# Optimization experiments

Measured on AMD Instinct MI355X. Metric: run time of the kernel, lower is better.

Reference implementation:

```python
import jax, jax.numpy as jnp
import numpy as np

B, S, D = 8, 1024, 512


def setup_inputs() -> dict:
    key = jax.random.key(0)
    k1, k2, k3, k4, k5, k6, k7 = jax.random.split(key, 7)
    inp = jax.random.normal(k1, (B, S, D), dtype=jnp.float32)
    aspect = jax.random.normal(k2, (B, S, D), dtype=jnp.float32)
    # lengths in [S//2, S], with max exactly S (the module requires max(len)==S)
    inp_len = jax.random.randint(k3, (B,), S // 2, S + 1).astype(jnp.float32)
    inp_len = inp_len.at[0].set(float(S))
    lim = float(np.sqrt(6.0 / (D + D)))  # xavier_uniform bound
    w1 = jax.random.uniform(k4, (D, D), jnp.float32, -lim, lim)
    b1 = jax.random.uniform(k5, (D,), jnp.float32, -lim, lim)
    w2 = jax.random.uniform(k6, (D, D), jnp.float32, -lim, lim)
    b2 = jax.random.uniform(k7, (D,), jnp.float32, -lim, lim)
    return {"inp": inp, "inp_len": inp_len, "aspect": aspect,
            "w1": w1, "b1": b1, "w2": w2, "b2": b2}


def reference(inp, inp_len, aspect, w1, b1, w2, b2):
    # inp, aspect: [B,S,D]; inp_len: [B] float lengths with max == S
    Bv, Sv, Dv = inp.shape
    scale = jnp.sqrt(inp_len)[:, None, None]                      # [B,1,1]
    att = jnp.einsum('bsd,btd->bst', aspect, inp) / scale          # [B,S,S]
    # mask over the query (row) dimension, as in the original expand
    mask = (jnp.arange(Sv)[None, :] < inp_len.astype(jnp.int32)[:, None]).astype(inp.dtype)  # [B,S]
    exp = att * mask[:, :, None]
    att_n = exp / (jnp.sum(exp, axis=-1, keepdims=True) + 1e-4)    # linear (non-exp) normalize
    weighted = jnp.einsum('bst,btd->bsd', att_n, inp)              # [B,S,D]
    ffn_inp = weighted + (inp + aspect) * mask[:, :, None]
    # FFN: two square linears with relu, plus inner residual
    o1 = jax.nn.relu(jnp.einsum('bsd,ed->bse', ffn_inp, w1) + b1)
    o2 = jax.nn.relu(jnp.einsum('bsd,ed->bse', o1, w2) + b2)
    ffn_out = o2 + ffn_inp
    final = ffn_inp + ffn_out
    return final / jnp.linalg.norm(final, axis=2, keepdims=True)
```

## Files before the change

kernel.cpp:

```cpp
#include <hip/hip_runtime.h>

#define Bq 8
#define Sq 1024
#define Dq 512

typedef __attribute__((ext_vector_type(8))) short bf16x8;
typedef __attribute__((ext_vector_type(4))) float f32x4;

__device__ __forceinline__ unsigned short f2bf(float f) {
  unsigned int u = __float_as_uint(f);
  return (unsigned short)((u + 0x7fffu + ((u >> 16) & 1u)) >> 16);
}

__device__ __forceinline__ void load_lds16(const unsigned short* g, unsigned short* l) {
  __builtin_amdgcn_global_load_lds(
      (const __attribute__((address_space(1))) unsigned int*)g,
      (__attribute__((address_space(3))) unsigned int*)l, 16, 0, 0);
}


__global__ __launch_bounds__(256) void prep_t(
    const float* __restrict__ inp,
    unsigned short* __restrict__ inpT, float* __restrict__ partial) {
  __shared__ unsigned short tile[64][66];
  __shared__ float csum[16][64];
  int idx = blockIdx.x;
  int tid = threadIdx.x;
  int b = idx & 7, tt = (idx >> 3) & 15, dd = idx >> 7;
  int r = tid >> 4, c4 = (tid & 15) * 4;
  const float* src = inp + ((size_t)b * Sq + tt * 64) * Dq + dd * 64;
  float cp0 = 0.f, cp1 = 0.f, cp2 = 0.f, cp3 = 0.f;
#pragma unroll
  for (int p = 0; p < 4; ++p) {
    float4 v = *(const float4*)(src + (size_t)(r + p * 16) * Dq + c4);
    ushort4 o; o.x = f2bf(v.x); o.y = f2bf(v.y); o.z = f2bf(v.z); o.w = f2bf(v.w);
    *(ushort4*)&tile[r + p * 16][c4] = o;
    cp0 += v.x; cp1 += v.y; cp2 += v.z; cp3 += v.w;
  }
  csum[r][c4] = cp0; csum[r][c4 + 1] = cp1; csum[r][c4 + 2] = cp2; csum[r][c4 + 3] = cp3;
  __syncthreads();
  unsigned short* dst = inpT + (size_t)b * Dq * Sq + (size_t)dd * 64 * Sq + tt * 64;
#pragma unroll
  for (int p = 0; p < 4; ++p) {
    int d = (tid >> 4) + p * 16;
    int tq = (tid & 15) * 4;
    ushort4 o;
    o.x = tile[tq][d]; o.y = tile[tq + 1][d]; o.z = tile[tq + 2][d]; o.w = tile[tq + 3][d];
    *(ushort4*)(dst + (size_t)d * Sq + tq) = o;
  }
  if (tid < 64) {
    float s = 0.f;
#pragma unroll
    for (int rr = 0; rr < 16; ++rr) s += csum[rr][tid];
    partial[((size_t)b * 16 + tt) * Dq + dd * 64 + tid] = s;
  }
}

__global__ __launch_bounds__(256, 5) void gram_fac(
    const unsigned short* __restrict__ inpT, const float* __restrict__ partial,
    const float* __restrict__ aspect, const float* __restrict__ lenv,
    const float* __restrict__ w1, const float* __restrict__ w2,
    unsigned short* __restrict__ Gm, float* __restrict__ fac,
    unsigned short* __restrict__ asp_bf,
    unsigned short* __restrict__ w1b, unsigned short* __restrict__ w2b) {
  __shared__ unsigned short sA[2][32 * 64];
  __shared__ unsigned short sB[2][64 * 64];
  int idx = blockIdx.x;
  int tid = threadIdx.x;
  int lane = tid & 63, wave = tid >> 6;

  if (idx >= 2048) {
    int blk = idx - 2048;
    const float* src = (blk < 256) ? w1 : w2;
    unsigned short* dst = (blk < 256) ? w1b : w2b;
    int li = ((blk & 255) * 256 + tid) * 4;
    int n = li >> 9, k = li & 511;
    float4 v = *(const float4*)(src + li);
    ushort4 o; o.x = f2bf(v.x); o.y = f2bf(v.y); o.z = f2bf(v.z); o.w = f2bf(v.w);
    int x = ((k >> 3) & 3) ^ ((n >> 1) & 3);
    int off = (k >> 5) * 16384 + n * 32 + x * 8 + (k & 7);
    *(ushort4*)(dst + off) = o;
    return;
  }
  if (idx >= 1536) {
    int blk = idx - 1536;
    const float* s = aspect + (size_t)blk * 8192 + tid * 4;
    unsigned short* d = asp_bf + (size_t)blk * 8192 + tid * 4;
#pragma unroll
    for (int j = 0; j < 8; ++j) {
      float4 v = *(const float4*)(s + j * 1024);
      ushort4 o; o.x = f2bf(v.x); o.y = f2bf(v.y); o.z = f2bf(v.z); o.w = f2bf(v.w);
      *(ushort4*)(d + j * 1024) = o;
    }
    return;
  }
  if (idx >= 1024) {
    float* cs = (float*)sA;
    int fblk = idx - 1024;
    int b = fblk >> 6;
    int s0 = (fblk & 63) * 16;
#pragma unroll
    for (int h = 0; h < 2; ++h) {
      int d = h * 256 + tid;
      float s = 0.f;
      const float* p = partial + (size_t)b * 16 * Dq + d;
#pragma unroll
      for (int t = 0; t < 16; ++t) s += p[t * Dq];
      cs[d] = s;
    }
    __syncthreads();
    int g = lane >> 4, lr = lane & 15;
    int row = s0 + wave * 4 + g;
    const float* a = aspect + ((size_t)b * Sq + row) * Dq + lr * 32;
    float sum = 0.f;
#pragma unroll
    for (int j = 0; j < 8; ++j) {
      float4 v = *(const float4*)(a + j * 4);
      const float* c = cs + lr * 32 + j * 4;
      sum += v.x * c[0] + v.y * c[1] + v.z * c[2] + v.w * c[3];
    }
#pragma unroll
    for (int off = 1; off < 16; off <<= 1) sum += __shfl_xor(sum, off, 64);
    if (lr == 0) {
      float len = lenv[b];
      float scale = sqrtf(len);
      float f = 0.f;
      if (row < (int)len) f = 1.f / (scale * (sum / scale + 1e-4f));
      fac[b * Sq + row] = f;
    }
    return;
  }

  const int K = 1024;
  int b = idx & 7;
  int tile = idx >> 3;
  int bm = tile & 15, bn = tile >> 4;
  const unsigned short* Ab = inpT + (size_t)b * Dq * Sq + (size_t)bm * 32 * K;
  const unsigned short* Bb = inpT + (size_t)b * Dq * Sq + (size_t)bn * 64 * K;
  int lr = lane & 15, lq = lane >> 4;
  int x7 = lr & 7;
  int l3 = lane >> 3, l7 = lane & 7;

  const unsigned short* gA = Ab + (size_t)(wave * 8 + l3) * K + (l7 ^ l3) * 8;
  const unsigned short* gB = Bb + (size_t)(wave * 16 + l3) * K + (l7 ^ l3) * 8;
  int dbaseA = (wave * 64 + lane) * 8;
  int dbaseB0 = (wave * 128 + lane) * 8;
  int dbaseB1 = (wave * 128 + 64 + lane) * 8;

  f32x4 acc[2] = {};

  auto issue = [&](int buf, int k0) {
    load_lds16(gA + k0, &sA[buf][dbaseA]);
    load_lds16(gB + k0, &sB[buf][dbaseB0]);
    load_lds16(gB + (size_t)8 * K + k0, &sB[buf][dbaseB1]);
  };

  int wm = (wave & 1) * 16, wn = (wave >> 1) * 32;
  issue(0, 0);
#pragma unroll
  for (int it = 0; it < 16; ++it) {
    int cur = it & 1;
    if (it + 1 < 16) {
      issue(cur ^ 1, (it + 1) << 6);
      asm volatile("s_waitcnt vmcnt(3)" ::: "memory");
    } else {
      asm volatile("s_waitcnt vmcnt(0)" ::: "memory");
    }
    __builtin_amdgcn_s_barrier();
#pragma unroll
    for (int c = 0; c < 2; ++c) {
      int g = c * 4 + lq;
      bf16x8 a0 = *(const bf16x8*)&sA[cur][((wm + lr) * 8 + (g ^ x7)) * 8];
      bf16x8 b0 = *(const bf16x8*)&sB[cur][((wn + lr) * 8 + (g ^ x7)) * 8];
      bf16x8 b1 = *(const bf16x8*)&sB[cur][((wn + 16 + lr) * 8 + (g ^ x7)) * 8];
      acc[0] = __builtin_amdgcn_mfma_f32_16x16x32_bf16(a0, b0, acc[0], 0, 0, 0);
      acc[1] = __builtin_amdgcn_mfma_f32_16x16x32_bf16(a0, b1, acc[1], 0, 0, 0);
    }
    asm volatile("s_waitcnt lgkmcnt(0)" ::: "memory");
    __builtin_amdgcn_sched_barrier(0);
    __builtin_amdgcn_s_barrier();
  }

  unsigned short* sP = sA[0];
#pragma unroll
  for (int ni = 0; ni < 2; ++ni)
#pragma unroll
    for (int i = 0; i < 4; ++i) {
      int rl = wm + lq * 4 + i;
      int ccl = wn + ni * 16 + lr;
      int x = (rl >> 3) ^ ((ccl >> 1) & 3);
      sP[ccl * 32 + x * 8 + (rl & 7)] = f2bf(acc[ni][i]);
    }
  __syncthreads();
  unsigned short* Ob = Gm + (size_t)b * 512 * 512 + (size_t)bm * 16384 + (size_t)bn * 2048;
  *(bf16x8*)(Ob + tid * 8) = *(const bf16x8*)(sP + tid * 8);
}

__global__ __launch_bounds__(512, 2) void mega_ffn(
    const unsigned short* __restrict__ aspb, const unsigned short* __restrict__ G,
    const unsigned short* __restrict__ w1b, const unsigned short* __restrict__ w2b,
    const float* __restrict__ b1, const float* __restrict__ b2,
    const float* __restrict__ inp, const float* __restrict__ aspect,
    const float* __restrict__ fac, const float* __restrict__ lenv,
    float* __restrict__ out) {
  __shared__ unsigned short ldsA[32 * 512];
  __shared__ float ssqW[8 * 32];
  int tid = threadIdx.x;
  int lane = tid & 63, wave = tid >> 6;
  int lr = lane & 15, lq = lane >> 4;
  int batch = blockIdx.x & 7;
  int pos = blockIdx.x >> 3;
  int r0 = batch * 1024 + pos * 32;
  int c0 = wave * 64;

  f32x4 acc[2][4];
  float ffnv[2][4][4];

  auto aoff = [&](int rr, int c) {
    int cq = c >> 3;
    return rr * 512 + ((cq ^ (rr & 7)) << 3) + (c & 7);
  };
  auto baddr = [&](const unsigned short* Bp, int kc, int cc) {
    return Bp + kc * 16384 + cc * 32 + ((lq ^ ((cc >> 1) & 3)) << 3);
  };

  auto gemmPhase = [&](const unsigned short* Bp) {
    bf16x8 bq[3][4];
    bf16x8 aq[2][2];
#pragma unroll
    for (int m = 0; m < 2; ++m)
#pragma unroll
      for (int t = 0; t < 4; ++t) acc[m][t] = (f32x4){0.f, 0.f, 0.f, 0.f};
#pragma unroll
    for (int t = 0; t < 4; ++t) {
      bq[0][t] = *(const bf16x8*)baddr(Bp, 0, c0 + t * 16 + lr);
      bq[1][t] = *(const bf16x8*)baddr(Bp, 1, c0 + t * 16 + lr);
    }
#pragma unroll
    for (int m = 0; m < 2; ++m)
      aq[0][m] = *(const bf16x8*)&ldsA[aoff(m * 16 + lr, lq * 8)];
#pragma unroll
    for (int kc = 0; kc < 16; ++kc) {
      if (kc + 2 < 16) {
#pragma unroll
        for (int t = 0; t < 4; ++t)
          bq[(kc + 2) % 3][t] = *(const bf16x8*)baddr(Bp, kc + 2, c0 + t * 16 + lr);
      }
      if (kc + 1 < 16) {
#pragma unroll
        for (int m = 0; m < 2; ++m)
          aq[(kc + 1) & 1][m] =
              *(const bf16x8*)&ldsA[aoff(m * 16 + lr, (kc + 1) * 32 + lq * 8)];
      }
      __builtin_amdgcn_s_setprio(1);
#pragma unroll
      for (int t = 0; t < 4; ++t) {
        acc[0][t] = __builtin_amdgcn_mfma_f32_16x16x32_bf16(aq[kc & 1][0], bq[kc % 3][t],
                                                            acc[0][t], 0, 0, 0);
        acc[1][t] = __builtin_amdgcn_mfma_f32_16x16x32_bf16(aq[kc & 1][1], bq[kc % 3][t],
                                                            acc[1][t], 0, 0, 0);
      }
      __builtin_amdgcn_s_setprio(0);
    }
  };

#pragma unroll
  for (int h = 0; h < 8; ++h) {
    int s = h * 512 + tid;
    int rr = s >> 6, sq = s & 63;
    int cq = sq ^ (rr & 7);
    load_lds16(aspb + (size_t)(r0 + rr) * 512 + cq * 8, ldsA + s * 8);
  }
  asm volatile("s_waitcnt vmcnt(0)" ::: "memory");
  __syncthreads();

  gemmPhase(G + (size_t)batch * 512 * 512);
  int len = (int)lenv[batch];
  float facv[2][4];
#pragma unroll
  for (int m = 0; m < 2; ++m)
#pragma unroll
    for (int i = 0; i < 4; ++i) facv[m][i] = fac[r0 + m * 16 + lq * 4 + i];
  __syncthreads();
#pragma unroll
  for (int m = 0; m < 2; ++m)
#pragma unroll
    for (int t = 0; t < 4; ++t)
#pragma unroll
      for (int i = 0; i < 4; ++i) {
        int rr = m * 16 + lq * 4 + i;
        int gr = r0 + rr;
        size_t idx = (size_t)gr * 512 + c0 + t * 16 + lr;
        float add = ((gr & 1023) < len) ? (inp[idx] + aspect[idx]) : 0.f;
        float v = acc[m][t][i] * facv[m][i] + add;
        ffnv[m][t][i] = v;
        ldsA[aoff(rr, c0 + t * 16 + lr)] = f2bf(v);
      }
  __syncthreads();

  gemmPhase(w1b);
  float biasv[4];
#pragma unroll
  for (int t = 0; t < 4; ++t) biasv[t] = b1[c0 + t * 16 + lr];
  __syncthreads();
#pragma unroll
  for (int m = 0; m < 2; ++m)
#pragma unroll
    for (int t = 0; t < 4; ++t)
#pragma unroll
      for (int i = 0; i < 4; ++i) {
        int rr = m * 16 + lq * 4 + i;
        ldsA[aoff(rr, c0 + t * 16 + lr)] = f2bf(fmaxf(acc[m][t][i] + biasv[t], 0.f));
      }
  __syncthreads();

  gemmPhase(w2b);
#pragma unroll
  for (int t = 0; t < 4; ++t) biasv[t] = b2[c0 + t * 16 + lr];
  float ssq[2][4] = {{0.f, 0.f, 0.f, 0.f}, {0.f, 0.f, 0.f, 0.f}};
#pragma unroll
  for (int m = 0; m < 2; ++m)
#pragma unroll
    for (int t = 0; t < 4; ++t)
#pragma unroll
      for (int i = 0; i < 4; ++i) {
        float v = 2.f * ffnv[m][t][i] + fmaxf(acc[m][t][i] + biasv[t], 0.f);
        ffnv[m][t][i] = v;
        ssq[m][i] += v * v;
      }
#pragma unroll
  for (int off = 1; off < 16; off <<= 1)
#pragma unroll
    for (int m = 0; m < 2; ++m)
#pragma unroll
      for (int i = 0; i < 4; ++i) ssq[m][i] += __shfl_xor(ssq[m][i], off, 64);
  if (lr == 0)
#pragma unroll
    for (int m = 0; m < 2; ++m)
#pragma unroll
      for (int i = 0; i < 4; ++i) ssqW[wave * 32 + m * 16 + lq * 4 + i] = ssq[m][i];
  __syncthreads();
  float rn[2][4];
#pragma unroll
  for (int m = 0; m < 2; ++m)
#pragma unroll
    for (int i = 0; i < 4; ++i) {
      float s = 0.f;
#pragma unroll
      for (int w = 0; w < 8; ++w) s += ssqW[w * 32 + m * 16 + lq * 4 + i];
      rn[m][i] = 1.f / sqrtf(s);
    }
#pragma unroll
  for (int m = 0; m < 2; ++m)
#pragma unroll
    for (int t = 0; t < 4; ++t)
#pragma unroll
      for (int i = 0; i < 4; ++i) {
        int gr = r0 + m * 16 + lq * 4 + i;
        out[(size_t)gr * 512 + c0 + t * 16 + lr] = ffnv[m][t][i] * rn[m][i];
      }
}

extern "C" void kernel_launch(void* const* d_in, const int* in_sizes, int n_in,
                              void* d_out, int out_size, void* d_ws, size_t ws_size,
                              hipStream_t stream) {
  const float* inp = (const float*)d_in[0];
  const float* inp_len = (const float*)d_in[1];
  const float* aspect = (const float*)d_in[2];
  const float* w1 = (const float*)d_in[3];
  const float* b1 = (const float*)d_in[4];
  const float* w2 = (const float*)d_in[5];
  const float* b2 = (const float*)d_in[6];
  float* out = (float*)d_out;

  char* W = (char*)d_ws;
  const size_t MB = 1ull << 20;
  unsigned short* asp_bf = (unsigned short*)(W + 0);
  unsigned short* inpT   = (unsigned short*)(W + 8 * MB);
  unsigned short* Gm     = (unsigned short*)(W + 16 * MB);
  unsigned short* w1bf   = (unsigned short*)(W + 20 * MB);
  unsigned short* w2bf   = (unsigned short*)(W + 20 * MB + 512 * 1024);
  float*          partial= (float*)(W + 21 * MB);
  float*          fac    = (float*)(W + 22 * MB);

  prep_t<<<1024, 256, 0, stream>>>(inp, inpT, partial);

  gram_fac<<<2560, 256, 0, stream>>>(inpT, partial, aspect, inp_len, w1, w2,
                                     Gm, fac, asp_bf, w1bf, w2bf);

  mega_ffn<<<256, 512, 0, stream>>>(
      asp_bf, Gm, w1bf, w2bf, b1, b2, inp, aspect, fac, inp_len, out);
}
```

Measured before the change: 130.3 us.

## Enlarge Gram GEMM tiles to 64x128 with 512-thread blocks and remap side tasks

```diff
diff --git a/kernel.cpp b/kernel.cpp
--- a/kernel.cpp
+++ b/kernel.cpp
@@ -56,24 +56,24 @@
   }
 }
 
-__global__ __launch_bounds__(256, 5) void gram_fac(
+__global__ __launch_bounds__(512, 2) void gram_fac(
     const unsigned short* __restrict__ inpT, const float* __restrict__ partial,
     const float* __restrict__ aspect, const float* __restrict__ lenv,
     const float* __restrict__ w1, const float* __restrict__ w2,
     unsigned short* __restrict__ Gm, float* __restrict__ fac,
     unsigned short* __restrict__ asp_bf,
     unsigned short* __restrict__ w1b, unsigned short* __restrict__ w2b) {
-  __shared__ unsigned short sA[2][32 * 64];
-  __shared__ unsigned short sB[2][64 * 64];
+  __shared__ unsigned short sA[2][64 * 64];
+  __shared__ unsigned short sB[2][128 * 64];
   int idx = blockIdx.x;
   int tid = threadIdx.x;
   int lane = tid & 63, wave = tid >> 6;
 
-  if (idx >= 2048) {
-    int blk = idx - 2048;
-    const float* src = (blk < 256) ? w1 : w2;
-    unsigned short* dst = (blk < 256) ? w1b : w2b;
-    int li = ((blk & 255) * 256 + tid) * 4;
+  if (idx >= 768) {
+    int blk = idx - 768;
+    const float* src = (blk < 128) ? w1 : w2;
+    unsigned short* dst = (blk < 128) ? w1b : w2b;
+    int li = ((blk & 127) * 512 + tid) * 4;
     int n = li >> 9, k = li & 511;
     float4 v = *(const float4*)(src + li);
     ushort4 o; o.x = f2bf(v.x); o.y = f2bf(v.y); o.z = f2bf(v.z); o.w = f2bf(v.w);
@@ -82,26 +82,25 @@
     *(ushort4*)(dst + off) = o;
     return;
   }
-  if (idx >= 1536) {
-    int blk = idx - 1536;
-    const float* s = aspect + (size_t)blk * 8192 + tid * 4;
-    unsigned short* d = asp_bf + (size_t)blk * 8192 + tid * 4;
+  if (idx >= 512) {
+    int blk = idx - 512;
+    const float* s = aspect + (size_t)blk * 16384 + tid * 4;
+    unsigned short* d = asp_bf + (size_t)blk * 16384 + tid * 4;
 #pragma unroll
     for (int j = 0; j < 8; ++j) {
-      float4 v = *(const float4*)(s + j * 1024);
+      float4 v = *(const float4*)(s + j * 2048);
       ushort4 o; o.x = f2bf(v.x); o.y = f2bf(v.y); o.z = f2bf(v.z); o.w = f2bf(v.w);
-      *(ushort4*)(d + j * 1024) = o;
+      *(ushort4*)(d + j * 2048) = o;
     }
     return;
   }
-  if (idx >= 1024) {
+  if (idx >= 256) {
     float* cs = (float*)sA;
-    int fblk = idx - 1024;
-    int b = fblk >> 6;
-    int s0 = (fblk & 63) * 16;
-#pragma unroll
-    for (int h = 0; h < 2; ++h) {
-      int d = h * 256 + tid;
+    int fblk = idx - 256;
+    int b = fblk >> 5;
+    int s0 = (fblk & 31) * 32;
+    {
+      int d = tid;
       float s = 0.f;
       const float* p = partial + (size_t)b * 16 * Dq + d;
 #pragma unroll
@@ -134,28 +133,27 @@
   const int K = 1024;
   int b = idx & 7;
   int tile = idx >> 3;
-  int bm = tile & 15, bn = tile >> 4;
-  const unsigned short* Ab = inpT + (size_t)b * Dq * Sq + (size_t)bm * 32 * K;
-  const unsigned short* Bb = inpT + (size_t)b * Dq * Sq + (size_t)bn * 64 * K;
+  int bm = tile & 7, bn = tile >> 3;
+  const unsigned short* Ab = inpT + (size_t)b * Dq * Sq + (size_t)bm * 64 * K;
+  const unsigned short* Bb = inpT + (size_t)b * Dq * Sq + (size_t)bn * 128 * K;
   int lr = lane & 15, lq = lane >> 4;
   int x7 = lr & 7;
-  int l3 = lane >> 3, l7 = lane & 7;
-
-  const unsigned short* gA = Ab + (size_t)(wave * 8 + l3) * K + (l7 ^ l3) * 8;
-  const unsigned short* gB = Bb + (size_t)(wave * 16 + l3) * K + (l7 ^ l3) * 8;
-  int dbaseA = (wave * 64 + lane) * 8;
-  int dbaseB0 = (wave * 128 + lane) * 8;
-  int dbaseB1 = (wave * 128 + 64 + lane) * 8;
-
-  f32x4 acc[2] = {};
+  int t8 = tid >> 3, t7 = tid & 7;
+
+  const unsigned short* gA = Ab + (size_t)t8 * K + (t7 ^ (t8 & 7)) * 8;
+  const unsigned short* gB = Bb + (size_t)t8 * K + (t7 ^ (t8 & 7)) * 8;
+  const unsigned short* gB2 = Bb + (size_t)(t8 + 64) * K + (t7 ^ (t8 & 7)) * 8;
+  int dbase = tid * 8;
+
+  f32x4 acc[2][2] = {};
 
   auto issue = [&](int buf, int k0) {
-    load_lds16(gA + k0, &sA[buf][dbaseA]);
-    load_lds16(gB + k0, &sB[buf][dbaseB0]);
-    load_lds16(gB + (size_t)8 * K + k0, &sB[buf][dbaseB1]);
+    load_lds16(gA + k0, &sA[buf][dbase]);
+    load_lds16(gB + k0, &sB[buf][dbase]);
+    load_lds16(gB2 + k0, &sB[buf][4096 + dbase]);
   };
 
-  int wm = (wave & 1) * 16, wn = (wave >> 1) * 32;
+  int wm = (wave & 1) * 32, wn = (wave >> 1) * 32;
   issue(0, 0);
 #pragma unroll
   for (int it = 0; it < 16; ++it) {
@@ -169,31 +167,40 @@
     __builtin_amdgcn_s_barrier();
 #pragma unroll
     for (int c = 0; c < 2; ++c) {
-      int g = c * 4 + lq;
-      bf16x8 a0 = *(const bf16x8*)&sA[cur][((wm + lr) * 8 + (g ^ x7)) * 8];
-      bf16x8 b0 = *(const bf16x8*)&sB[cur][((wn + lr) * 8 + (g ^ x7)) * 8];
-      bf16x8 b1 = *(const bf16x8*)&sB[cur][((wn + 16 + lr) * 8 + (g ^ x7)) * 8];
-      acc[0] = __builtin_amdgcn_mfma_f32_16x16x32_bf16(a0, b0, acc[0], 0, 0, 0);
-      acc[1] = __builtin_amdgcn_mfma_f32_16x16x32_bf16(a0, b1, acc[1], 0, 0, 0);
+      int g = (c * 4 + lq) ^ x7;
+      bf16x8 a0 = *(const bf16x8*)&sA[cur][((wm + lr) * 8 + g) * 8];
+      bf16x8 a1 = *(const bf16x8*)&sA[cur][((wm + 16 + lr) * 8 + g) * 8];
+      bf16x8 b0 = *(const bf16x8*)&sB[cur][((wn + lr) * 8 + g) * 8];
+      bf16x8 b1 = *(const bf16x8*)&sB[cur][((wn + 16 + lr) * 8 + g) * 8];
+      acc[0][0] = __builtin_amdgcn_mfma_f32_16x16x32_bf16(a0, b0, acc[0][0], 0, 0, 0);
+      acc[0][1] = __builtin_amdgcn_mfma_f32_16x16x32_bf16(a0, b1, acc[0][1], 0, 0, 0);
+      acc[1][0] = __builtin_amdgcn_mfma_f32_16x16x32_bf16(a1, b0, acc[1][0], 0, 0, 0);
+      acc[1][1] = __builtin_amdgcn_mfma_f32_16x16x32_bf16(a1, b1, acc[1][1], 0, 0, 0);
     }
     asm volatile("s_waitcnt lgkmcnt(0)" ::: "memory");
     __builtin_amdgcn_sched_barrier(0);
     __builtin_amdgcn_s_barrier();
   }
 
-  unsigned short* sP = sA[0];
-#pragma unroll
-  for (int ni = 0; ni < 2; ++ni)
-#pragma unroll
-    for (int i = 0; i < 4; ++i) {
-      int rl = wm + lq * 4 + i;
-      int ccl = wn + ni * 16 + lr;
-      int x = (rl >> 3) ^ ((ccl >> 1) & 3);
-      sP[ccl * 32 + x * 8 + (rl & 7)] = f2bf(acc[ni][i]);
-    }
-  __syncthreads();
-  unsigned short* Ob = Gm + (size_t)b * 512 * 512 + (size_t)bm * 16384 + (size_t)bn * 2048;
-  *(bf16x8*)(Ob + tid * 8) = *(const bf16x8*)(sP + tid * 8);
+  unsigned short* sP = sB[0];
+  int kcl = wm >> 5;
+#pragma unroll
+  for (int mi = 0; mi < 2; ++mi)
+#pragma unroll
+    for (int ni = 0; ni < 2; ++ni)
+#pragma unroll
+      for (int i = 0; i < 4; ++i) {
+        int rl = mi * 16 + lq * 4 + i;
+        int nl = wn + ni * 16 + lr;
+        int x = (rl >> 3) ^ ((nl >> 1) & 3);
+        sP[kcl * 4096 + nl * 32 + x * 8 + (rl & 7)] = f2bf(acc[mi][ni][i]);
+      }
+  __syncthreads();
+  unsigned short* Ob = Gm + (size_t)b * 512 * 512 + (size_t)(bm * 2) * 16384 +
+                       (size_t)bn * 4096;
+#pragma unroll
+  for (int h = 0; h < 2; ++h)
+    *(bf16x8*)(Ob + h * 16384 + tid * 8) = *(const bf16x8*)(sP + h * 4096 + tid * 8);
 }
 
 __global__ __launch_bounds__(512, 2) void mega_ffn(
@@ -385,7 +392,7 @@
 
   prep_t<<<1024, 256, 0, stream>>>(inp, inpT, partial);
 
-  gram_fac<<<2560, 256, 0, stream>>>(inpT, partial, aspect, inp_len, w1, w2,
+  gram_fac<<<1024, 512, 0, stream>>>(inpT, partial, aspect, inp_len, w1, w2,
                                      Gm, fac, asp_bf, w1bf, w2bf);
 
   mega_ffn<<<256, 512, 0, stream>>>(
```

Result: no change. 132.1 us (+1.3%).

## Stage FFN weight tiles through a triple-buffered LDS ring via async loads

Applied to the files above, without the earlier changes.

```diff
diff --git a/kernel.cpp b/kernel.cpp
--- a/kernel.cpp
+++ b/kernel.cpp
@@ -196,15 +196,19 @@
   *(bf16x8*)(Ob + tid * 8) = *(const bf16x8*)(sP + tid * 8);
 }
 
-__global__ __launch_bounds__(512, 2) void mega_ffn(
+#define MEGA_SMEM (32768 + 3 * 32768 + 1024)
+
+__global__ __launch_bounds__(512, 1) void mega_ffn(
     const unsigned short* __restrict__ aspb, const unsigned short* __restrict__ G,
     const unsigned short* __restrict__ w1b, const unsigned short* __restrict__ w2b,
     const float* __restrict__ b1, const float* __restrict__ b2,
     const float* __restrict__ inp, const float* __restrict__ aspect,
     const float* __restrict__ fac, const float* __restrict__ lenv,
     float* __restrict__ out) {
-  __shared__ unsigned short ldsA[32 * 512];
-  __shared__ float ssqW[8 * 32];
+  extern __shared__ char smem[];
+  unsigned short* ldsA = (unsigned short*)smem;
+  unsigned short* wbuf = (unsigned short*)(smem + 32768);
+  float* ssqW = (float*)(smem + 32768 + 3 * 32768);
   int tid = threadIdx.x;
   int lane = tid & 63, wave = tid >> 6;
   int lr = lane & 15, lq = lane >> 4;
@@ -220,52 +224,52 @@
     int cq = c >> 3;
     return rr * 512 + ((cq ^ (rr & 7)) << 3) + (c & 7);
   };
-  auto baddr = [&](const unsigned short* Bp, int kc, int cc) {
-    return Bp + kc * 16384 + cc * 32 + ((lq ^ ((cc >> 1) & 3)) << 3);
+  int bx = (lq ^ ((lr >> 1) & 3)) * 8;
+  int rdbase = (c0 + lr) * 32 + bx;
+
+  auto stage = [&](int buf, int kc, const unsigned short* Bp) {
+    const unsigned short* src = Bp + kc * 16384 + wave * 2048 + lane * 8;
+    unsigned short* dst = wbuf + buf * 16384 + wave * 2048 + lane * 8;
+#pragma unroll
+    for (int i = 0; i < 4; ++i) load_lds16(src + i * 512, dst + i * 512);
   };
 
   auto gemmPhase = [&](const unsigned short* Bp) {
-    bf16x8 bq[3][4];
-    bf16x8 aq[2][2];
 #pragma unroll
     for (int m = 0; m < 2; ++m)
 #pragma unroll
       for (int t = 0; t < 4; ++t) acc[m][t] = (f32x4){0.f, 0.f, 0.f, 0.f};
-#pragma unroll
-    for (int t = 0; t < 4; ++t) {
-      bq[0][t] = *(const bf16x8*)baddr(Bp, 0, c0 + t * 16 + lr);
-      bq[1][t] = *(const bf16x8*)baddr(Bp, 1, c0 + t * 16 + lr);
-    }
-#pragma unroll
-    for (int m = 0; m < 2; ++m)
-      aq[0][m] = *(const bf16x8*)&ldsA[aoff(m * 16 + lr, lq * 8)];
+    stage(0, 0, Bp);
+    stage(1, 1, Bp);
 #pragma unroll
     for (int kc = 0; kc < 16; ++kc) {
-      if (kc + 2 < 16) {
-#pragma unroll
-        for (int t = 0; t < 4; ++t)
-          bq[(kc + 2) % 3][t] = *(const bf16x8*)baddr(Bp, kc + 2, c0 + t * 16 + lr);
-      }
-      if (kc + 1 < 16) {
-#pragma unroll
-        for (int m = 0; m < 2; ++m)
-          aq[(kc + 1) & 1][m] =
-              *(const bf16x8*)&ldsA[aoff(m * 16 + lr, (kc + 1) * 32 + lq * 8)];
-      }
+      int cur = kc % 3;
+      if (kc + 2 < 16) stage((kc + 2) % 3, kc + 2, Bp);
+      if (kc < 14) {
+        asm volatile("s_waitcnt vmcnt(8)" ::: "memory");
+      } else if (kc == 14) {
+        asm volatile("s_waitcnt vmcnt(4)" ::: "memory");
+      } else {
+        asm volatile("s_waitcnt vmcnt(0)" ::: "memory");
+      }
+      bf16x8 a0 = *(const bf16x8*)&ldsA[aoff(lr, kc * 32 + lq * 8)];
+      bf16x8 a1 = *(const bf16x8*)&ldsA[aoff(16 + lr, kc * 32 + lq * 8)];
+      bf16x8 bfr[4];
+#pragma unroll
+      for (int t = 0; t < 4; ++t)
+        bfr[t] = *(const bf16x8*)&wbuf[cur * 16384 + rdbase + t * 512];
       __builtin_amdgcn_s_setprio(1);
 #pragma unroll
       for (int t = 0; t < 4; ++t) {
-        acc[0][t] = __builtin_amdgcn_mfma_f32_16x16x32_bf16(aq[kc & 1][0], bq[kc % 3][t],
-                                                            acc[0][t], 0, 0, 0);
-        acc[1][t] = __builtin_amdgcn_mfma_f32_16x16x32_bf16(aq[kc & 1][1], bq[kc % 3][t],
-                                                            acc[1][t], 0, 0, 0);
+        acc[0][t] = __builtin_amdgcn_mfma_f32_16x16x32_bf16(a0, bfr[t], acc[0][t], 0, 0, 0);
+        acc[1][t] = __builtin_amdgcn_mfma_f32_16x16x32_bf16(a1, bfr[t], acc[1][t], 0, 0, 0);
       }
       __builtin_amdgcn_s_setprio(0);
     }
   };
 
 #pragma unroll
-  for (int h = 0; h < 8; ++h) {
+  for (int h = 0; h < 4; ++h) {
     int s = h * 512 + tid;
     int rr = s >> 6, sq = s & 63;
     int cq = sq ^ (rr & 7);
@@ -388,6 +392,8 @@
   gram_fac<<<2560, 256, 0, stream>>>(inpT, partial, aspect, inp_len, w1, w2,
                                      Gm, fac, asp_bf, w1bf, w2bf);
 
-  mega_ffn<<<256, 512, 0, stream>>>(
+  hipFuncSetAttribute((const void*)mega_ffn,
+                      hipFuncAttributeMaxDynamicSharedMemorySize, MEGA_SMEM);
+  mega_ffn<<<256, 512, MEGA_SMEM, stream>>>(
       asp_bf, Gm, w1bf, w2bf, b1, b2, inp, aspect, fac, inp_len, out);
 }
```

Measured after the change: 132.0 us. Within noise of the previous version (+1.3%).
